# Performance work log

Hardware: AMD Instinct MI355X
Metric: run time of the kernel (lower is better)

## Reference

```python
import jax, jax.numpy as jnp
import numpy as np

N, E, D, L = 50000, 800000, 256, 3  # nodes, edges, feature dim, layers


def setup_inputs() -> dict:
    key = jax.random.key(0)
    k = jax.random.split(key, 5)
    edge_index = jax.random.randint(k[0], (2, E), 0, N)  # row0=src, row1=tgt (PyG COO)
    x_init = jax.random.normal(k[1], (N, D), dtype=jnp.float32)
    s = 1.0 / np.sqrt(D).astype(np.float32)  # Glorot-ish init scale
    W_l = jax.random.uniform(k[2], (L, D, D), minval=-s, maxval=s, dtype=jnp.float32)
    W_r = jax.random.uniform(k[3], (L, D, D), minval=-s, maxval=s, dtype=jnp.float32)
    b = jnp.zeros((L, D), dtype=jnp.float32)
    return {"edge_index": edge_index, "x_init": x_init, "W_l": W_l, "W_r": W_r, "b": b}


def reference(edge_index, x_init, W_l, W_r, b):
    src, tgt = edge_index[0], edge_index[1]
    # mean-aggregation normalizer, computed once (degree of each target node)
    deg = jax.ops.segment_sum(jnp.ones((E,), jnp.float32), tgt, num_segments=N)
    inv_deg = jnp.where(deg > 0, 1.0 / deg, 0.0)[:, None]  # [N,1]

    def sage_conv(x, i):
        # PyG SAGEConv (aggr='mean'): out = lin_l(mean_j x_j) + lin_r(x_i)
        agg = jax.ops.segment_sum(x[src], tgt, num_segments=N) * inv_deg  # [N,D]
        return agg @ W_l[i] + x @ W_r[i] + b[i]

    x = x_init
    x_list = []
    for i in range(L - 1):
        x = jax.nn.relu(sage_conv(x, i) + x)  # residual then ReLU
        x_list.append(x)
        # dropout p=0.0 -> identity
    x = sage_conv(x, L - 1) + x  # final layer with residual, no ReLU
    x_list.append(x)
    return jnp.concatenate(x_list, axis=1)  # [N, L*D] concat of all layer outputs
```

## Files before the change

kernel.cpp:

```cpp
#include <hip/hip_runtime.h>
#include <hip/hip_bf16.h>
#include <stdint.h>

#define NN 50000
#define EE 800000
#define DD 256
#define LL 3
#define NBLK 49
#define NPAD 50176

using floatx4 = __attribute__((ext_vector_type(4))) float;
using shortx8 = __attribute__((ext_vector_type(8))) short;

union U8 { shortx8 v; uint32_t u[4]; };

typedef __attribute__((address_space(1))) const unsigned int gu32;
typedef __attribute__((address_space(3))) unsigned int lu32;
__device__ __forceinline__ void async_copy16(const void* g, void* l) {
    __builtin_amdgcn_global_load_lds((gu32*)g, (lu32*)l, 16, 0, 0);
}

__device__ __forceinline__ uint16_t f2bf(float f) {
    __hip_bfloat16 h = __float2bfloat16(f);
    return *reinterpret_cast<uint16_t*>(&h);
}
__device__ __forceinline__ float bf2f(uint32_t u) {
    union { uint32_t u32; float f; } cv; cv.u32 = (u & 0xffffu) << 16; return cv.f;
}

__global__ void k_count(const int* __restrict__ tgt, int* __restrict__ deg) {
    int e = blockIdx.x * 256 + threadIdx.x;
    if (e < EE) atomicAdd(&deg[tgt[e]], 1);
}

__global__ void k_scan1(const int* __restrict__ deg, int* __restrict__ row_start,
                        int* __restrict__ bsum) {
    __shared__ int wsum[16];
    int t = threadIdx.x, w = t >> 6, lane = t & 63;
    int i = blockIdx.x * 1024 + t;
    int v = (i < NN) ? deg[i] : 0;
    int s = v;
#pragma unroll
    for (int off = 1; off < 64; off <<= 1) {
        int u = __shfl_up(s, off);
        if (lane >= off) s += u;
    }
    if (lane == 63) wsum[w] = s;
    __syncthreads();
    if (t < 16) {
        int ws = wsum[t];
#pragma unroll
        for (int off = 1; off < 16; off <<= 1) {
            int u = __shfl_up(ws, off);
            if (t >= off) ws += u;
        }
        wsum[t] = ws;
    }
    __syncthreads();
    int off = (w > 0) ? wsum[w - 1] : 0;
    if (i < NN) row_start[i] = off + s - v;
    if (t == 1023) bsum[blockIdx.x] = off + s;
}

__global__ void k_scan2(int* __restrict__ bsum, int* __restrict__ row_start) {
    int t = threadIdx.x;
    int v = (t < NBLK) ? bsum[t] : 0;
    int s = v;
#pragma unroll
    for (int off = 1; off < 64; off <<= 1) {
        int u = __shfl_up(s, off);
        if (t >= off) s += u;
    }
    if (t < NBLK) bsum[t] = s - v;
    if (t == 0) row_start[NN] = EE;
}

__global__ void k_init2(const int* __restrict__ deg, const int* __restrict__ bsum,
                        int* __restrict__ row_start, int* __restrict__ cursor,
                        float* __restrict__ invd) {
    int i = blockIdx.x * 1024 + threadIdx.x;
    if (i < NN) {
        int r = row_start[i] + bsum[blockIdx.x];
        row_start[i] = r;
        cursor[i] = r;
        int d = deg[i];
        invd[i] = d > 0 ? 1.0f / (float)d : 0.0f;
    }
}

__global__ void k_scatter(const int* __restrict__ src, const int* __restrict__ tgt,
                          int* __restrict__ cursor, int* __restrict__ csr) {
    int e = blockIdx.x * 256 + threadIdx.x;
    if (e < EE) {
        int p = atomicAdd(&cursor[tgt[e]], 1);
        csr[p] = src[e];
    }
}

__global__ void k_wprep(const float* __restrict__ Wl, const float* __restrict__ Wr,
                        uint16_t* __restrict__ wtl_hi, uint16_t* __restrict__ wtl_lo,
                        uint16_t* __restrict__ wtr_hi, uint16_t* __restrict__ wtr_lo) {
    int d = blockIdx.x * 256 + threadIdx.x;
    int i = d >> 16, n = (d >> 8) & 255, k = d & 255;
    int s = (i << 16) | (k << 8) | n;
    float wl = Wl[s], wr = Wr[s];
    uint32_t ul = __float_as_uint(wl), ur = __float_as_uint(wr);
    wtl_hi[d] = (uint16_t)(ul >> 16);
    wtl_lo[d] = f2bf(wl - __uint_as_float(ul & 0xFFFF0000u));
    wtr_hi[d] = (uint16_t)(ur >> 16);
    wtr_lo[d] = f2bf(wr - __uint_as_float(ur & 0xFFFF0000u));
}

__global__ void k_split0(const float* __restrict__ x, uint16_t* __restrict__ xs2) {
    int t = threadIdx.x;
    int row = blockIdx.x * 4 + (t >> 6);
    int col = (t & 63) * 4;
    uint32_t h01 = 0, h23 = 0, l01 = 0, l23 = 0;
    if (row < NN) {
        float4 v = *reinterpret_cast<const float4*>(x + (size_t)row * DD + col);
        uint32_t u0 = __float_as_uint(v.x), u1 = __float_as_uint(v.y);
        uint32_t u2 = __float_as_uint(v.z), u3 = __float_as_uint(v.w);
        h01 = (u0 >> 16) | (u1 & 0xFFFF0000u);
        h23 = (u2 >> 16) | (u3 & 0xFFFF0000u);
        l01 = (uint32_t)f2bf(v.x - __uint_as_float(u0 & 0xFFFF0000u))
            | ((uint32_t)f2bf(v.y - __uint_as_float(u1 & 0xFFFF0000u)) << 16);
        l23 = (uint32_t)f2bf(v.z - __uint_as_float(u2 & 0xFFFF0000u))
            | ((uint32_t)f2bf(v.w - __uint_as_float(u3 & 0xFFFF0000u)) << 16);
    }
    *reinterpret_cast<uint2*>(xs2 + (size_t)row * 512 + col) = make_uint2(h01, h23);
    *reinterpret_cast<uint2*>(xs2 + (size_t)row * 512 + 256 + col) = make_uint2(l01, l23);
}

__global__ __launch_bounds__(256, 2) void k_gemm4(
    const uint16_t* __restrict__ xs2,
    const uint16_t* __restrict__ whl, const uint16_t* __restrict__ whr,
    const uint16_t* __restrict__ wll, const uint16_t* __restrict__ wlr,
    uint16_t* __restrict__ yl, float* __restrict__ outz)
{
    extern __shared__ __align__(16) char smem[];
    int t = threadIdx.x;
    int wave = t >> 6, lane = t & 63, quad = lane >> 4, l16 = lane & 15;
    int row0 = (blockIdx.x >> 3) * 256, col0 = (blockIdx.x & 7) * 32;

    {
        const uint16_t* mp0 = whl + col0 * 256;
        const uint16_t* mp1 = whr + col0 * 256;
        const uint16_t* mp2 = wll + col0 * 256;
        const uint16_t* mp3 = wlr + col0 * 256;
        int nrow = t >> 5;
        int soff = ((t & 31) ^ nrow) * 8;
#pragma unroll
        for (int i = 0; i < 4; ++i) {
            int go = (i * 8 + nrow) * 256 + soff;
            char* d = smem + i * 4096 + t * 16;
            async_copy16(mp0 + go, d);
            async_copy16(mp1 + go, d + 16384);
            async_copy16(mp2 + go, d + 32768);
            async_copy16(mp3 + go, d + 49152);
        }
    }

    const uint16_t* ap[4];
#pragma unroll
    for (int rt = 0; rt < 4; ++rt)
        ap[rt] = xs2 + (size_t)(row0 + wave * 64 + rt * 16 + l16) * 512 + quad * 8;

    floatx4 accy[4][2], accz[4][2];
#pragma unroll
    for (int rt = 0; rt < 4; ++rt)
#pragma unroll
        for (int ct = 0; ct < 2; ++ct) {
            accy[rt][ct] = (floatx4){0.f, 0.f, 0.f, 0.f};
            accz[rt][ct] = (floatx4){0.f, 0.f, 0.f, 0.f};
        }

    U8 abuf[2][4];
#pragma unroll
    for (int rt = 0; rt < 4; ++rt)
        abuf[0][rt].v = *reinterpret_cast<const shortx8*>(ap[rt]);

    __syncthreads();

    int bbase0 = l16 * 512;
    int bbase1 = (16 + l16) * 512;
    int bxor = l16 & 7;

#pragma unroll
    for (int c = 0; c < 16; ++c) {
        if (c < 15) {
#pragma unroll
            for (int rt = 0; rt < 4; ++rt)
                abuf[(c + 1) & 1][rt].v =
                    *reinterpret_cast<const shortx8*>(ap[rt] + (c + 1) * 32);
        }
        int kk = c & 7;
        int so = ((kk * 4 + quad) ^ bxor) * 16;
        shortx8 b00 = *reinterpret_cast<const shortx8*>(smem + bbase0 + so);
        shortx8 b10 = *reinterpret_cast<const shortx8*>(smem + bbase1 + so);
        shortx8 b01 = *reinterpret_cast<const shortx8*>(smem + 16384 + bbase0 + so);
        shortx8 b11 = *reinterpret_cast<const shortx8*>(smem + 16384 + bbase1 + so);
        shortx8 c00, c10, c01, c11;
        if (c < 8) {
            c00 = *reinterpret_cast<const shortx8*>(smem + 32768 + bbase0 + so);
            c10 = *reinterpret_cast<const shortx8*>(smem + 32768 + bbase1 + so);
            c01 = *reinterpret_cast<const shortx8*>(smem + 49152 + bbase0 + so);
            c11 = *reinterpret_cast<const shortx8*>(smem + 49152 + bbase1 + so);
        }
#pragma unroll
        for (int rt = 0; rt < 4; ++rt) {
            shortx8 a = abuf[c & 1][rt].v;
            accy[rt][0] = __builtin_amdgcn_mfma_f32_16x16x32_bf16(a, b00, accy[rt][0], 0, 0, 0);
            accy[rt][1] = __builtin_amdgcn_mfma_f32_16x16x32_bf16(a, b10, accy[rt][1], 0, 0, 0);
            accz[rt][0] = __builtin_amdgcn_mfma_f32_16x16x32_bf16(a, b01, accz[rt][0], 0, 0, 0);
            accz[rt][1] = __builtin_amdgcn_mfma_f32_16x16x32_bf16(a, b11, accz[rt][1], 0, 0, 0);
            if (c < 8) {
                accy[rt][0] = __builtin_amdgcn_mfma_f32_16x16x32_bf16(a, c00, accy[rt][0], 0, 0, 0);
                accy[rt][1] = __builtin_amdgcn_mfma_f32_16x16x32_bf16(a, c10, accy[rt][1], 0, 0, 0);
                accz[rt][0] = __builtin_amdgcn_mfma_f32_16x16x32_bf16(a, c01, accz[rt][0], 0, 0, 0);
                accz[rt][1] = __builtin_amdgcn_mfma_f32_16x16x32_bf16(a, c11, accz[rt][1], 0, 0, 0);
            }
        }
    }

#pragma unroll
    for (int rt = 0; rt < 4; ++rt) {
#pragma unroll
        for (int ct = 0; ct < 2; ++ct) {
            int colg = col0 + ct * 16 + l16;
#pragma unroll
            for (int r = 0; r < 4; ++r) {
                int rowg = row0 + wave * 64 + rt * 16 + quad * 4 + r;
                if (rowg < NN) {
                    yl[(size_t)rowg * 256 + colg] = f2bf(accy[rt][ct][r]);
                    outz[(size_t)rowg * (LL * DD) + colg] = accz[rt][ct][r];
                }
            }
        }
    }
}

__global__ __launch_bounds__(256) void k_finish(
    const int* __restrict__ rs, const int* __restrict__ csr,
    const float* __restrict__ invd, const uint16_t* __restrict__ yl,
    uint16_t* __restrict__ xs2, const float* __restrict__ bias,
    float* __restrict__ outz, int do_relu, int wsplit)
{
    int node = blockIdx.x * 4 + (threadIdx.x >> 6);
    int lane = threadIdx.x & 63;
    int col = lane * 4;
    int s = rs[node], e = rs[node + 1];
    float a0 = 0.f, a1 = 0.f, a2 = 0.f, a3 = 0.f;
    int p = s;
    for (; p + 4 <= e; p += 4) {
        int i0 = csr[p], i1 = csr[p + 1], i2 = csr[p + 2], i3 = csr[p + 3];
        uint2 v0 = *reinterpret_cast<const uint2*>(yl + (size_t)i0 * 256 + col);
        uint2 v1 = *reinterpret_cast<const uint2*>(yl + (size_t)i1 * 256 + col);
        uint2 v2 = *reinterpret_cast<const uint2*>(yl + (size_t)i2 * 256 + col);
        uint2 v3 = *reinterpret_cast<const uint2*>(yl + (size_t)i3 * 256 + col);
        a0 += (bf2f(v0.x) + bf2f(v1.x)) + (bf2f(v2.x) + bf2f(v3.x));
        a1 += (bf2f(v0.x >> 16) + bf2f(v1.x >> 16)) + (bf2f(v2.x >> 16) + bf2f(v3.x >> 16));
        a2 += (bf2f(v0.y) + bf2f(v1.y)) + (bf2f(v2.y) + bf2f(v3.y));
        a3 += (bf2f(v0.y >> 16) + bf2f(v1.y >> 16)) + (bf2f(v2.y >> 16) + bf2f(v3.y >> 16));
    }
    for (; p < e; ++p) {
        int i = csr[p];
        uint2 v = *reinterpret_cast<const uint2*>(yl + (size_t)i * 256 + col);
        a0 += bf2f(v.x); a1 += bf2f(v.x >> 16); a2 += bf2f(v.y); a3 += bf2f(v.y >> 16);
    }
    float w = invd[node];
    float* zp = outz + (size_t)node * (LL * DD) + col;
    float4 z = *reinterpret_cast<const float4*>(zp);
    float4 b = *reinterpret_cast<const float4*>(bias + col);
    uint2 xh = *reinterpret_cast<const uint2*>(xs2 + (size_t)node * 512 + col);
    uint2 xl = *reinterpret_cast<const uint2*>(xs2 + (size_t)node * 512 + 256 + col);
    float o0 = z.x + b.x + (bf2f(xh.x) + bf2f(xl.x)) + w * a0;
    float o1 = z.y + b.y + (bf2f(xh.x >> 16) + bf2f(xl.x >> 16)) + w * a1;
    float o2 = z.z + b.z + (bf2f(xh.y) + bf2f(xl.y)) + w * a2;
    float o3 = z.w + b.w + (bf2f(xh.y >> 16) + bf2f(xl.y >> 16)) + w * a3;
    if (do_relu) {
        o0 = fmaxf(o0, 0.f); o1 = fmaxf(o1, 0.f);
        o2 = fmaxf(o2, 0.f); o3 = fmaxf(o3, 0.f);
    }
    *reinterpret_cast<float4*>(zp) = make_float4(o0, o1, o2, o3);
    if (wsplit) {
        uint32_t u0 = __float_as_uint(o0), u1 = __float_as_uint(o1);
        uint32_t u2 = __float_as_uint(o2), u3 = __float_as_uint(o3);
        uint32_t h01 = (u0 >> 16) | (u1 & 0xFFFF0000u);
        uint32_t h23 = (u2 >> 16) | (u3 & 0xFFFF0000u);
        uint32_t l01 = (uint32_t)f2bf(o0 - __uint_as_float(u0 & 0xFFFF0000u))
                     | ((uint32_t)f2bf(o1 - __uint_as_float(u1 & 0xFFFF0000u)) << 16);
        uint32_t l23 = (uint32_t)f2bf(o2 - __uint_as_float(u2 & 0xFFFF0000u))
                     | ((uint32_t)f2bf(o3 - __uint_as_float(u3 & 0xFFFF0000u)) << 16);
        *reinterpret_cast<uint2*>(xs2 + (size_t)node * 512 + col) = make_uint2(h01, h23);
        *reinterpret_cast<uint2*>(xs2 + (size_t)node * 512 + 256 + col) = make_uint2(l01, l23);
    }
}

extern "C" void kernel_launch(void* const* d_in, const int* in_sizes, int n_in,
                              void* d_out, int out_size, void* d_ws, size_t ws_size,
                              hipStream_t stream) {
    const int*   edge   = (const int*)d_in[0];
    const float* x_init = (const float*)d_in[1];
    const float* W_l    = (const float*)d_in[2];
    const float* W_r    = (const float*)d_in[3];
    const float* bias   = (const float*)d_in[4];
    float*       out    = (float*)d_out;

    char* ws = (char*)d_ws;
    int*      degI      = (int*)(ws + 0x0000000);
    int*      row_start = (int*)(ws + 0x0040000);
    int*      cursor    = (int*)(ws + 0x0080000);
    float*    invd      = (float*)(ws + 0x00C0000);
    int*      bsum      = (int*)(ws + 0x0100000);
    int*      csr       = (int*)(ws + 0x0140000);
    uint16_t* whl       = (uint16_t*)(ws + 0x0480000);
    uint16_t* whr       = (uint16_t*)(ws + 0x04E0000);
    uint16_t* wll       = (uint16_t*)(ws + 0x0540000);
    uint16_t* wlr       = (uint16_t*)(ws + 0x05A0000);
    uint16_t* yl        = (uint16_t*)(ws + 0x0600000);
    uint16_t* xs2       = (uint16_t*)(ws + 0x1E80000);

    hipMemsetAsync(degI, 0, NN * sizeof(int), stream);
    k_count<<<(EE + 255) / 256, 256, 0, stream>>>(edge + EE, degI);
    k_scan1<<<NBLK, 1024, 0, stream>>>(degI, row_start, bsum);
    k_scan2<<<1, 64, 0, stream>>>(bsum, row_start);
    k_init2<<<NBLK, 1024, 0, stream>>>(degI, bsum, row_start, cursor, invd);
    k_scatter<<<(EE + 255) / 256, 256, 0, stream>>>(edge, edge + EE, cursor, csr);
    k_wprep<<<(LL * DD * DD) / 256, 256, 0, stream>>>(W_l, W_r, whl, wll, whr, wlr);
    k_split0<<<NPAD / 4, 256, 0, stream>>>(x_init, xs2);

    for (int i = 0; i < LL; ++i) {
        size_t wo = (size_t)i * DD * DD;
        k_gemm4<<<(NPAD / 256) * 8, 256, 65536, stream>>>(
            xs2, whl + wo, whr + wo, wll + wo, wlr + wo,
            yl, out + (size_t)i * DD);
        k_finish<<<NN / 4, 256, 0, stream>>>(
            row_start, csr, invd, yl, xs2, bias + (size_t)i * DD,
            out + (size_t)i * DD, (i < LL - 1) ? 1 : 0, (i < LL - 1) ? 1 : 0);
    }
}
```

Measured before the change: 746.8 us.

## Fold residual into W_r identity, bias into GEMM epilogue, deepen prefetch and gather unroll

Adds the identity to W_r so the GEMM computes the residual term directly, and adds the bias in the GEMM epilogue. This lets k_finish skip reading the split x and the bias. The GEMM grid is remapped to a column-major block order (200 row groups per column, 4 of them idle), and the A-operand prefetch goes from double to triple buffering. k_finish also gains an 8-wide gather unroll and loads z earlier. Folding the residual into bf16 hi/lo weights slightly changes rounding, and the deeper prefetch and unroll add register pressure.

Measured after the change: 716.0 us. 4.1% less time.

```diff
diff --git a/kernel.cpp b/kernel.cpp
--- a/kernel.cpp
+++ b/kernel.cpp
@@ -103,7 +103,8 @@
     int d = blockIdx.x * 256 + threadIdx.x;
     int i = d >> 16, n = (d >> 8) & 255, k = d & 255;
     int s = (i << 16) | (k << 8) | n;
-    float wl = Wl[s], wr = Wr[s];
+    float wl = Wl[s];
+    float wr = Wr[s] + ((n == k) ? 1.0f : 0.0f);
     uint32_t ul = __float_as_uint(wl), ur = __float_as_uint(wr);
     wtl_hi[d] = (uint16_t)(ul >> 16);
     wtl_lo[d] = f2bf(wl - __uint_as_float(ul & 0xFFFF0000u));
@@ -135,12 +136,17 @@
     const uint16_t* __restrict__ xs2,
     const uint16_t* __restrict__ whl, const uint16_t* __restrict__ whr,
     const uint16_t* __restrict__ wll, const uint16_t* __restrict__ wlr,
+    const float* __restrict__ bias,
     uint16_t* __restrict__ yl, float* __restrict__ outz)
 {
     extern __shared__ __align__(16) char smem[];
+    int bid = blockIdx.x;
+    int cg = bid / 200;
+    int rg = bid - cg * 200;
+    if (rg >= 196) return;
     int t = threadIdx.x;
     int wave = t >> 6, lane = t & 63, quad = lane >> 4, l16 = lane & 15;
-    int row0 = (blockIdx.x >> 3) * 256, col0 = (blockIdx.x & 7) * 32;
+    int row0 = rg * 256, col0 = cg * 32;
 
     {
         const uint16_t* mp0 = whl + col0 * 256;
@@ -174,10 +180,12 @@
             accz[rt][ct] = (floatx4){0.f, 0.f, 0.f, 0.f};
         }
 
-    U8 abuf[2][4];
-#pragma unroll
-    for (int rt = 0; rt < 4; ++rt)
+    U8 abuf[3][4];
+#pragma unroll
+    for (int rt = 0; rt < 4; ++rt) {
         abuf[0][rt].v = *reinterpret_cast<const shortx8*>(ap[rt]);
+        abuf[1][rt].v = *reinterpret_cast<const shortx8*>(ap[rt] + 32);
+    }
 
     __syncthreads();
 
@@ -187,11 +195,11 @@
 
 #pragma unroll
     for (int c = 0; c < 16; ++c) {
-        if (c < 15) {
+        if (c < 14) {
 #pragma unroll
             for (int rt = 0; rt < 4; ++rt)
-                abuf[(c + 1) & 1][rt].v =
-                    *reinterpret_cast<const shortx8*>(ap[rt] + (c + 1) * 32);
+                abuf[(c + 2) % 3][rt].v =
+                    *reinterpret_cast<const shortx8*>(ap[rt] + (c + 2) * 32);
         }
         int kk = c & 7;
         int so = ((kk * 4 + quad) ^ bxor) * 16;
@@ -208,7 +216,7 @@
         }
 #pragma unroll
         for (int rt = 0; rt < 4; ++rt) {
-            shortx8 a = abuf[c & 1][rt].v;
+            shortx8 a = abuf[c % 3][rt].v;
             accy[rt][0] = __builtin_amdgcn_mfma_f32_16x16x32_bf16(a, b00, accy[rt][0], 0, 0, 0);
             accy[rt][1] = __builtin_amdgcn_mfma_f32_16x16x32_bf16(a, b10, accy[rt][1], 0, 0, 0);
             accz[rt][0] = __builtin_amdgcn_mfma_f32_16x16x32_bf16(a, b01, accz[rt][0], 0, 0, 0);
@@ -222,6 +230,7 @@
         }
     }
 
+    float bct[2] = { bias[col0 + l16], bias[col0 + 16 + l16] };
 #pragma unroll
     for (int rt = 0; rt < 4; ++rt) {
 #pragma unroll
@@ -232,7 +241,7 @@
                 int rowg = row0 + wave * 64 + rt * 16 + quad * 4 + r;
                 if (rowg < NN) {
                     yl[(size_t)rowg * 256 + colg] = f2bf(accy[rt][ct][r]);
-                    outz[(size_t)rowg * (LL * DD) + colg] = accz[rt][ct][r];
+                    outz[(size_t)rowg * (LL * DD) + colg] = accz[rt][ct][r] + bct[ct];
                 }
             }
         }
@@ -242,15 +251,38 @@
 __global__ __launch_bounds__(256) void k_finish(
     const int* __restrict__ rs, const int* __restrict__ csr,
     const float* __restrict__ invd, const uint16_t* __restrict__ yl,
-    uint16_t* __restrict__ xs2, const float* __restrict__ bias,
-    float* __restrict__ outz, int do_relu, int wsplit)
+    uint16_t* __restrict__ xs2, float* __restrict__ outz,
+    int do_relu, int wsplit)
 {
     int node = blockIdx.x * 4 + (threadIdx.x >> 6);
     int lane = threadIdx.x & 63;
     int col = lane * 4;
     int s = rs[node], e = rs[node + 1];
+    float w = invd[node];
+    float* zp = outz + (size_t)node * (LL * DD) + col;
+    float4 z = *reinterpret_cast<const float4*>(zp);
     float a0 = 0.f, a1 = 0.f, a2 = 0.f, a3 = 0.f;
     int p = s;
+    for (; p + 8 <= e; p += 8) {
+        int i0 = csr[p],     i1 = csr[p + 1], i2 = csr[p + 2], i3 = csr[p + 3];
+        int i4 = csr[p + 4], i5 = csr[p + 5], i6 = csr[p + 6], i7 = csr[p + 7];
+        uint2 v0 = *reinterpret_cast<const uint2*>(yl + (size_t)i0 * 256 + col);
+        uint2 v1 = *reinterpret_cast<const uint2*>(yl + (size_t)i1 * 256 + col);
+        uint2 v2 = *reinterpret_cast<const uint2*>(yl + (size_t)i2 * 256 + col);
+        uint2 v3 = *reinterpret_cast<const uint2*>(yl + (size_t)i3 * 256 + col);
+        uint2 v4 = *reinterpret_cast<const uint2*>(yl + (size_t)i4 * 256 + col);
+        uint2 v5 = *reinterpret_cast<const uint2*>(yl + (size_t)i5 * 256 + col);
+        uint2 v6 = *reinterpret_cast<const uint2*>(yl + (size_t)i6 * 256 + col);
+        uint2 v7 = *reinterpret_cast<const uint2*>(yl + (size_t)i7 * 256 + col);
+        a0 += ((bf2f(v0.x) + bf2f(v1.x)) + (bf2f(v2.x) + bf2f(v3.x)))
+            + ((bf2f(v4.x) + bf2f(v5.x)) + (bf2f(v6.x) + bf2f(v7.x)));
+        a1 += ((bf2f(v0.x >> 16) + bf2f(v1.x >> 16)) + (bf2f(v2.x >> 16) + bf2f(v3.x >> 16)))
+            + ((bf2f(v4.x >> 16) + bf2f(v5.x >> 16)) + (bf2f(v6.x >> 16) + bf2f(v7.x >> 16)));
+        a2 += ((bf2f(v0.y) + bf2f(v1.y)) + (bf2f(v2.y) + bf2f(v3.y)))
+            + ((bf2f(v4.y) + bf2f(v5.y)) + (bf2f(v6.y) + bf2f(v7.y)));
+        a3 += ((bf2f(v0.y >> 16) + bf2f(v1.y >> 16)) + (bf2f(v2.y >> 16) + bf2f(v3.y >> 16)))
+            + ((bf2f(v4.y >> 16) + bf2f(v5.y >> 16)) + (bf2f(v6.y >> 16) + bf2f(v7.y >> 16)));
+    }
     for (; p + 4 <= e; p += 4) {
         int i0 = csr[p], i1 = csr[p + 1], i2 = csr[p + 2], i3 = csr[p + 3];
         uint2 v0 = *reinterpret_cast<const uint2*>(yl + (size_t)i0 * 256 + col);
@@ -267,16 +299,10 @@
         uint2 v = *reinterpret_cast<const uint2*>(yl + (size_t)i * 256 + col);
         a0 += bf2f(v.x); a1 += bf2f(v.x >> 16); a2 += bf2f(v.y); a3 += bf2f(v.y >> 16);
     }
-    float w = invd[node];
-    float* zp = outz + (size_t)node * (LL * DD) + col;
-    float4 z = *reinterpret_cast<const float4*>(zp);
-    float4 b = *reinterpret_cast<const float4*>(bias + col);
-    uint2 xh = *reinterpret_cast<const uint2*>(xs2 + (size_t)node * 512 + col);
-    uint2 xl = *reinterpret_cast<const uint2*>(xs2 + (size_t)node * 512 + 256 + col);
-    float o0 = z.x + b.x + (bf2f(xh.x) + bf2f(xl.x)) + w * a0;
-    float o1 = z.y + b.y + (bf2f(xh.x >> 16) + bf2f(xl.x >> 16)) + w * a1;
-    float o2 = z.z + b.z + (bf2f(xh.y) + bf2f(xl.y)) + w * a2;
-    float o3 = z.w + b.w + (bf2f(xh.y >> 16) + bf2f(xl.y >> 16)) + w * a3;
+    float o0 = z.x + w * a0;
+    float o1 = z.y + w * a1;
+    float o2 = z.z + w * a2;
+    float o3 = z.w + w * a3;
     if (do_relu) {
         o0 = fmaxf(o0, 0.f); o1 = fmaxf(o1, 0.f);
         o2 = fmaxf(o2, 0.f); o3 = fmaxf(o3, 0.f);
@@ -331,11 +357,11 @@
 
     for (int i = 0; i < LL; ++i) {
         size_t wo = (size_t)i * DD * DD;
-        k_gemm4<<<(NPAD / 256) * 8, 256, 65536, stream>>>(
-            xs2, whl + wo, whr + wo, wll + wo, wlr + wo,
+        k_gemm4<<<1600, 256, 65536, stream>>>(
+            xs2, whl + wo, whr + wo, wll + wo, wlr + wo, bias + (size_t)i * DD,
             yl, out + (size_t)i * DD);
         k_finish<<<NN / 4, 256, 0, stream>>>(
-            row_start, csr, invd, yl, xs2, bias + (size_t)i * DD,
+            row_start, csr, invd, yl, xs2,
             out + (size_t)i * DD, (i < LL - 1) ? 1 : 0, (i < LL - 1) ? 1 : 0);
     }
 }
```
